# Kernel optimization log

Hardware: AMD Instinct MI355X
Metric: run time of the kernel (lower is better)

## Reference

```python
import jax, jax.numpy as jnp
import numpy as np

D_MODEL = 1024
D_FF = 4096
N_HEADS = 16
D_K = D_MODEL // N_HEADS
EPS = 1e-6
NEG_INF = 1.0e9


def _layer_norm(x, g, b):
    mu = jnp.mean(x, axis=-1, keepdims=True)
    var = jnp.mean(jnp.square(x - mu), axis=-1, keepdims=True)
    return (x - mu) / jnp.sqrt(var + EPS) * g + b


def setup_inputs() -> dict:
    key = jax.random.key(0)
    ks = jax.random.split(key, 16)
    s = 1.0 / np.sqrt(D_MODEL)
    inp = {
        'x': jax.random.normal(ks[0], (4, 2048, D_MODEL), dtype=jnp.float32),
        'e_mask': jnp.ones((4, 1, 2048), dtype=jnp.int32),
        'ln1_g': jnp.ones((D_MODEL,), jnp.float32),
        'ln1_b': jnp.zeros((D_MODEL,), jnp.float32),
        'wq': jax.random.normal(ks[1], (D_MODEL, D_MODEL), jnp.float32) * s,
        'bq': jnp.zeros((D_MODEL,), jnp.float32),
        'wk': jax.random.normal(ks[2], (D_MODEL, D_MODEL), jnp.float32) * s,
        'bk': jnp.zeros((D_MODEL,), jnp.float32),
        'wv': jax.random.normal(ks[3], (D_MODEL, D_MODEL), jnp.float32) * s,
        'bv': jnp.zeros((D_MODEL,), jnp.float32),
        'w0': jax.random.normal(ks[4], (D_MODEL, D_MODEL), jnp.float32) * s,
        'b0': jnp.zeros((D_MODEL,), jnp.float32),
        'ln2_g': jnp.ones((D_MODEL,), jnp.float32),
        'ln2_b': jnp.zeros((D_MODEL,), jnp.float32),
        'w1': jax.random.normal(ks[5], (D_MODEL, D_FF), jnp.float32) * s,
        'b1': jnp.zeros((D_FF,), jnp.float32),
        'w2': jax.random.normal(ks[6], (D_FF, D_MODEL), jnp.float32) * (1.0 / np.sqrt(D_FF)),
        'b2': jnp.zeros((D_MODEL,), jnp.float32),
    }
    return inp


def reference(x, e_mask, ln1_g, ln1_b, wq, bq, wk, bk, wv, bv, w0, b0,
              ln2_g, ln2_b, w1, b1, w2, b2):
    B, S, _ = x.shape
    # --- pre-LN multihead attention (dropout = identity in eval) ---
    x1 = _layer_norm(x, ln1_g, ln1_b)
    q = (x1 @ wq + bq).reshape(B, S, N_HEADS, D_K).transpose(0, 2, 1, 3)
    k = (x1 @ wk + bk).reshape(B, S, N_HEADS, D_K).transpose(0, 2, 1, 3)
    v = (x1 @ wv + bv).reshape(B, S, N_HEADS, D_K).transpose(0, 2, 1, 3)
    scores = jnp.einsum('bhqd,bhkd->bhqk', q, k) / np.sqrt(D_K).astype(np.float32)
    mask = e_mask[:, None, :, :]  # [B,1,1,S] broadcast over heads and queries
    scores = jnp.where(mask == 0, -NEG_INF, scores)
    attn = jax.nn.softmax(scores, axis=-1)
    ctx = jnp.einsum('bhqk,bhkd->bhqd', attn, v)
    ctx = ctx.transpose(0, 2, 1, 3).reshape(B, S, D_MODEL)
    x = x + (ctx @ w0 + b0)
    # --- pre-LN feed-forward ---
    x2 = _layer_norm(x, ln2_g, ln2_b)
    h = jax.nn.relu(x2 @ w1 + b1)
    x = x + (h @ w2 + b2)
    return x
```

## Files before the change

kernel.cpp:

```cpp
#include <hip/hip_runtime.h>
#include <cstdint>
#include <cstddef>

typedef __bf16 bf16;
typedef __bf16 bf16x8 __attribute__((ext_vector_type(8)));
typedef __bf16 bf16x4 __attribute__((ext_vector_type(4)));
typedef float  f32x4  __attribute__((ext_vector_type(4)));
typedef float  f32x16 __attribute__((ext_vector_type(16)));

#define D_MODEL 1024
#define D_FF    4096
#define SEQ     2048
#define NB      4
#define NH      16
#define DKH     64
#define MTOT    (NB * SEQ)

__device__ __forceinline__ void gl_lds16(const void* g, void* l) {
  __builtin_amdgcn_global_load_lds(
      (__attribute__((address_space(1))) unsigned int*)(void*)g,
      (__attribute__((address_space(3))) unsigned int*)l, 16, 0, 0);
}

__device__ __forceinline__ unsigned cvtpk(float lo, float hi_) {
  unsigned r;
  asm("v_cvt_pk_bf16_f32 %0, %1, %2" : "=v"(r) : "v"(lo), "v"(hi_));
  return r;
}
__device__ __forceinline__ void pl32swap(unsigned& a, unsigned& b) {
  asm volatile("v_permlane32_swap_b32 %0, %1" : "+v"(a), "+v"(b));
}

__global__ __launch_bounds__(256) void k_transp(const float* __restrict__ W,
                                                bf16* __restrict__ Wt, int R, int C) {
  __shared__ float tile[32][33];
  const int c0 = blockIdx.x * 32, r0 = blockIdx.y * 32;
  const int t = threadIdx.x;
  const int rl = t >> 5, cl = t & 31;
#pragma unroll
  for (int i = 0; i < 4; ++i)
    tile[rl + i * 8][cl] = W[(size_t)(r0 + rl + i * 8) * C + c0 + cl];
  __syncthreads();
#pragma unroll
  for (int i = 0; i < 4; ++i)
    Wt[(size_t)(c0 + rl + i * 8) * R + r0 + cl] = (bf16)tile[cl][rl + i * 8];
}

__global__ __launch_bounds__(256) void k_ln(const float* __restrict__ x,
                                            const float* __restrict__ g,
                                            const float* __restrict__ b,
                                            bf16* __restrict__ out) {
  const int row = blockIdx.x;
  const int t = threadIdx.x;
  const float4 v = ((const float4*)(x + (size_t)row * D_MODEL))[t];
  float s  = v.x + v.y + v.z + v.w;
  float s2 = v.x * v.x + v.y * v.y + v.z * v.z + v.w * v.w;
#pragma unroll
  for (int off = 1; off < 64; off <<= 1) {
    s  += __shfl_xor(s, off);
    s2 += __shfl_xor(s2, off);
  }
  __shared__ float red[8];
  const int wv = t >> 6;
  if ((t & 63) == 0) { red[wv] = s; red[4 + wv] = s2; }
  __syncthreads();
  s  = red[0] + red[1] + red[2] + red[3];
  s2 = red[4] + red[5] + red[6] + red[7];
  const float mu   = s * (1.f / D_MODEL);
  const float var  = s2 * (1.f / D_MODEL) - mu * mu;
  const float rstd = rsqrtf(var + 1e-6f);
  const float4 gv = ((const float4*)g)[t];
  const float4 bv = ((const float4*)b)[t];
  bf16x4 o;
  o[0] = (bf16)((v.x - mu) * rstd * gv.x + bv.x);
  o[1] = (bf16)((v.y - mu) * rstd * gv.y + bv.y);
  o[2] = (bf16)((v.z - mu) * rstd * gv.z + bv.z);
  o[3] = (bf16)((v.w - mu) * rstd * gv.w + bv.w);
  *(bf16x4*)(out + (size_t)row * D_MODEL + t * 4) = o;
}

template <int EPI>
__global__ __launch_bounds__(512, 2) void k_gemm(
    const bf16* __restrict__ A, const bf16* __restrict__ Bt,
    const float* __restrict__ bias, const float* __restrict__ biasK,
    const float* __restrict__ biasV, float alpha,
    bf16* __restrict__ obf, float* __restrict__ of32,
    const float* __restrict__ resid,
    int M, int N, int K) {
  __shared__ char lds[2][65536];
  const int t = threadIdx.x, lane = t & 63, w = t >> 6;
  const int wm = w >> 2, wn = w & 3;

  const int gx = gridDim.x;
  const int nwg = gx * gridDim.y;
  int id = blockIdx.x + blockIdx.y * gx;
  id = (id & 7) * (nwg >> 3) + (id >> 3);
  const int tn = (id % gx) * 256;
  const int tm = (id / gx) * 256;

  const int scol = 8 * ((lane & 7) ^ (lane >> 3));
  const bf16* aS[4];
  const bf16* bS[4];
#pragma unroll
  for (int i = 0; i < 4; ++i) {
    aS[i] = A  + (size_t)(tm + 8 * (w + 8 * i) + (lane >> 3)) * K + scol;
    bS[i] = Bt + (size_t)(tn + 8 * (w + 8 * i) + (lane >> 3)) * K + scol;
  }
  const int dA = w * 1024;
  const int dB = 32768 + w * 1024;

  const int rA = (wm * 128 + (lane & 15)) * 128;
  const int rB = 32768 + (wn * 64 + (lane & 15)) * 128;
  const int cS0 = (((lane >> 4) * 16)     ) ^ ((lane & 7) << 4);
  const int cS1 = (64 + ((lane >> 4) * 16)) ^ ((lane & 7) << 4);

  f32x4 acc[8][4] = {};
  const int KT = K >> 6;

#pragma unroll
  for (int i = 0; i < 4; ++i) {
    gl_lds16(aS[i], lds[0] + dA + i * 8192);
    gl_lds16(bS[i], lds[0] + dB + i * 8192);
  }
  gl_lds16(aS[0] + 64, lds[1] + dA);
  gl_lds16(aS[1] + 64, lds[1] + dA + 8192);
  asm volatile("s_waitcnt vmcnt(2)" ::: "memory");
  __builtin_amdgcn_s_barrier();
  __builtin_amdgcn_sched_barrier(0);

#define RD(buf, off) (*(const bf16x8*)((buf) + (off)))

  for (int tt = 0; tt < KT; ++tt) {
    char* bufc = lds[tt & 1];
    char* bufn = lds[(tt & 1) ^ 1];
    const int k1 = (tt + 1 < KT ? tt + 1 : KT - 1) * 64;
    const int k2 = (tt + 2 < KT ? tt + 2 : KT - 1) * 64;
    bf16x8 a0[4][2], a1[4][2], b[4][2];
#pragma unroll
    for (int m = 0; m < 4; ++m) {
      a0[m][0] = RD(bufc, rA + m * 2048 + cS0);
      a0[m][1] = RD(bufc, rA + m * 2048 + cS1);
    }
#pragma unroll
    for (int n = 0; n < 2; ++n) {
      b[n][0] = RD(bufc, rB + n * 2048 + cS0);
      b[n][1] = RD(bufc, rB + n * 2048 + cS1);
    }
    gl_lds16(aS[2] + k1, bufn + dA + 2 * 8192);
    gl_lds16(aS[3] + k1, bufn + dA + 3 * 8192);
    gl_lds16(bS[0] + k1, bufn + dB);
    __builtin_amdgcn_s_setprio(1);
#pragma unroll
    for (int m = 0; m < 4; ++m)
#pragma unroll
      for (int n = 0; n < 2; ++n)
#pragma unroll
        for (int s = 0; s < 2; ++s)
          acc[m][n] = __builtin_amdgcn_mfma_f32_16x16x32_bf16(a0[m][s], b[n][s], acc[m][n], 0, 0, 0);
    __builtin_amdgcn_s_setprio(0);
#pragma unroll
    for (int n = 2; n < 4; ++n) {
      b[n][0] = RD(bufc, rB + n * 2048 + cS0);
      b[n][1] = RD(bufc, rB + n * 2048 + cS1);
    }
#pragma unroll
    for (int m = 0; m < 4; ++m) {
      a1[m][0] = RD(bufc, rA + (4 + m) * 2048 + cS0);
      a1[m][1] = RD(bufc, rA + (4 + m) * 2048 + cS1);
    }
    gl_lds16(bS[1] + k1, bufn + dB + 8192);
    gl_lds16(bS[2] + k1, bufn + dB + 2 * 8192);
    gl_lds16(bS[3] + k1, bufn + dB + 3 * 8192);
    __builtin_amdgcn_s_setprio(1);
#pragma unroll
    for (int m = 0; m < 4; ++m)
#pragma unroll
      for (int n = 2; n < 4; ++n)
#pragma unroll
        for (int s = 0; s < 2; ++s)
          acc[m][n] = __builtin_amdgcn_mfma_f32_16x16x32_bf16(a0[m][s], b[n][s], acc[m][n], 0, 0, 0);
    __builtin_amdgcn_s_setprio(0);
    asm volatile("s_waitcnt lgkmcnt(0)" ::: "memory");
    __builtin_amdgcn_s_barrier();
    __builtin_amdgcn_sched_barrier(0);
    gl_lds16(aS[0] + k2, bufc + dA);
    gl_lds16(aS[1] + k2, bufc + dA + 8192);
    __builtin_amdgcn_s_setprio(1);
#pragma unroll
    for (int m = 0; m < 4; ++m)
#pragma unroll
      for (int n = 0; n < 2; ++n)
#pragma unroll
        for (int s = 0; s < 2; ++s)
          acc[4 + m][n] = __builtin_amdgcn_mfma_f32_16x16x32_bf16(a1[m][s], b[n][s], acc[4 + m][n], 0, 0, 0);
    __builtin_amdgcn_s_setprio(0);
    __builtin_amdgcn_s_setprio(1);
#pragma unroll
    for (int m = 0; m < 4; ++m)
#pragma unroll
      for (int n = 2; n < 4; ++n)
#pragma unroll
        for (int s = 0; s < 2; ++s)
          acc[4 + m][n] = __builtin_amdgcn_mfma_f32_16x16x32_bf16(a1[m][s], b[n][s], acc[4 + m][n], 0, 0, 0);
    __builtin_amdgcn_s_setprio(0);
    asm volatile("s_waitcnt vmcnt(2)" ::: "memory");
    __builtin_amdgcn_s_barrier();
    __builtin_amdgcn_sched_barrier(0);
  }
#undef RD
  asm volatile("s_waitcnt vmcnt(0)" ::: "memory");

  const int row0 = tm + wm * 128 + (lane >> 4) * 4;
  const int col0 = tn + wn * 64 + (lane & 15);
  const int which = tn >> 10;
  const float* bp = (EPI == 1) ? (which == 0 ? bias : (which == 1 ? biasK : biasV)) : bias;
  const float af_ = (EPI == 1) ? (which == 0 ? alpha : 1.f) : alpha;
  bf16* qkvB = (EPI == 1) ? obf + (size_t)which * MTOT * D_MODEL : obf;
#pragma unroll
  for (int n = 0; n < 4; ++n) {
    const int col = col0 + n * 16;
    const float bv = (EPI == 1) ? bp[col & 1023] : bp[col];
#pragma unroll
    for (int m = 0; m < 8; ++m) {
#pragma unroll
      for (int r = 0; r < 4; ++r) {
        const int row = row0 + m * 16 + r;
        float val = acc[m][n][r] + bv;
        if constexpr (EPI == 1) {
          const int bb = row >> 11, ss = row & 2047, hh = (col >> 6) & 15, dd = col & 63;
          qkvB[(((size_t)bb * NH + hh) * SEQ + ss) * DKH + dd] = (bf16)(val * af_);
        } else if constexpr (EPI == 2) {
          const size_t idx = (size_t)row * N + col;
          of32[idx] = resid[idx] + val;
        } else {
          obf[(size_t)row * N + col] = (bf16)fmaxf(val, 0.f);
        }
      }
    }
  }
}

template <int EPI>
__global__ __launch_bounds__(512, 2) void k_gemmB(
    const bf16* __restrict__ A, const bf16* __restrict__ Bt,
    const float* __restrict__ bias, float alpha,
    bf16* __restrict__ obf, float* __restrict__ of32,
    const float* __restrict__ resid,
    int M, int N, int K) {
  __shared__ char lds[2][49152];
  const int t = threadIdx.x, lane = t & 63, w = t >> 6;
  const int wm = w >> 1, wn = w & 1;

  const int gx = gridDim.x;
  const int nwg = gx * gridDim.y;
  int id = blockIdx.x + blockIdx.y * gx;
  id = (id & 7) * (nwg >> 3) + (id >> 3);
  const int tn = (id % gx) * 128;
  const int tm = (id / gx) * 256;

  const int srow = w * 16 + (lane >> 3);
  const int scol = 8 * ((lane & 7) ^ (lane >> 3));
  const bf16* aS = A  + (size_t)(tm + srow) * K + scol;
  const bf16* bS = Bt + (size_t)(tn + srow) * K + scol;
  const int dstOff = w * 2048;

  const int rA = (wm * 64 + (lane & 15)) * 128;
  const int rB = 32768 + (wn * 64 + (lane & 15)) * 128;
  const int cS0 = (((lane >> 4) * 16)      ) ^ ((lane & 7) << 4);
  const int cS1 = (64 + ((lane >> 4) * 16) ) ^ ((lane & 7) << 4);

  f32x4 acc[4][4] = {};
  const int KT = K >> 6;

  gl_lds16(aS,                 lds[0] + dstOff);
  gl_lds16(aS + 8 * K,         lds[0] + dstOff + 1024);
  gl_lds16(aS + 128 * K,       lds[0] + 16384 + dstOff);
  gl_lds16(aS + 136 * K,       lds[0] + 16384 + dstOff + 1024);
  gl_lds16(bS,                 lds[0] + 32768 + dstOff);
  gl_lds16(bS + 8 * K,         lds[0] + 32768 + dstOff + 1024);
  gl_lds16(aS + 64,            lds[1] + dstOff);
  gl_lds16(aS + 8 * K + 64,    lds[1] + dstOff + 1024);
  asm volatile("s_waitcnt vmcnt(2)" ::: "memory");
  __builtin_amdgcn_s_barrier();
  __builtin_amdgcn_sched_barrier(0);

#define RD(buf, off) (*(const bf16x8*)((buf) + (off)))
#define MM(m, n, s) acc[m][n] = __builtin_amdgcn_mfma_f32_16x16x32_bf16(a[m][s], b[n][s], acc[m][n], 0, 0, 0)

  for (int tt = 0; tt < KT; ++tt) {
    char* bufc = lds[tt & 1];
    char* bufn = lds[(tt & 1) ^ 1];
    const int k1 = (tt + 1 < KT ? tt + 1 : KT - 1) * 64;
    const int k2 = (tt + 2 < KT ? tt + 2 : KT - 1) * 64;
    bf16x8 a[4][2], b[4][2];
    a[0][0] = RD(bufc, rA + cS0);          a[0][1] = RD(bufc, rA + cS1);
    a[1][0] = RD(bufc, rA + 2048 + cS0);   a[1][1] = RD(bufc, rA + 2048 + cS1);
    b[0][0] = RD(bufc, rB + cS0);
    b[1][0] = RD(bufc, rB + 2048 + cS0);
    b[2][0] = RD(bufc, rB + 4096 + cS0);
    b[3][0] = RD(bufc, rB + 6144 + cS0);
    gl_lds16(aS + 128 * K + k1, bufn + 16384 + dstOff);
    gl_lds16(aS + 136 * K + k1, bufn + 16384 + dstOff + 1024);
    __builtin_amdgcn_s_setprio(1);
    MM(0,0,0); MM(0,1,0); MM(0,2,0); MM(0,3,0);
    MM(1,0,0); MM(1,1,0); MM(1,2,0); MM(1,3,0);
    __builtin_amdgcn_s_setprio(0);
    a[2][0] = RD(bufc, rA + 4096 + cS0);   a[2][1] = RD(bufc, rA + 4096 + cS1);
    a[3][0] = RD(bufc, rA + 6144 + cS0);   a[3][1] = RD(bufc, rA + 6144 + cS1);
    b[0][1] = RD(bufc, rB + cS1);
    b[1][1] = RD(bufc, rB + 2048 + cS1);
    b[2][1] = RD(bufc, rB + 4096 + cS1);
    b[3][1] = RD(bufc, rB + 6144 + cS1);
    gl_lds16(bS + k1,         bufn + 32768 + dstOff);
    gl_lds16(bS + 8 * K + k1, bufn + 32768 + dstOff + 1024);
    __builtin_amdgcn_s_setprio(1);
    MM(2,0,0); MM(2,1,0); MM(2,2,0); MM(2,3,0);
    MM(3,0,0); MM(3,1,0); MM(3,2,0); MM(3,3,0);
    __builtin_amdgcn_s_setprio(0);
    asm volatile("s_waitcnt lgkmcnt(0)" ::: "memory");
    __builtin_amdgcn_s_barrier();
    __builtin_amdgcn_sched_barrier(0);
    gl_lds16(aS + k2,         bufc + dstOff);
    gl_lds16(aS + 8 * K + k2, bufc + dstOff + 1024);
    __builtin_amdgcn_s_setprio(1);
    MM(0,0,1); MM(0,1,1); MM(0,2,1); MM(0,3,1);
    MM(1,0,1); MM(1,1,1); MM(1,2,1); MM(1,3,1);
    __builtin_amdgcn_s_setprio(0);
    __builtin_amdgcn_s_setprio(1);
    MM(2,0,1); MM(2,1,1); MM(2,2,1); MM(2,3,1);
    MM(3,0,1); MM(3,1,1); MM(3,2,1); MM(3,3,1);
    __builtin_amdgcn_s_setprio(0);
    asm volatile("s_waitcnt vmcnt(2)" ::: "memory");
    __builtin_amdgcn_s_barrier();
    __builtin_amdgcn_sched_barrier(0);
  }
#undef RD
#undef MM
  asm volatile("s_waitcnt vmcnt(0)" ::: "memory");

  const int row0 = tm + wm * 64 + (lane >> 4) * 4;
  const int col0 = tn + wn * 64 + (lane & 15);
#pragma unroll
  for (int n = 0; n < 4; ++n) {
    const int col = col0 + n * 16;
    const float bv = bias[col];
#pragma unroll
    for (int m = 0; m < 4; ++m) {
#pragma unroll
      for (int r = 0; r < 4; ++r) {
        const int row = row0 + m * 16 + r;
        float val = acc[m][n][r] + bv;
        if constexpr (EPI == 2) {
          const size_t idx = (size_t)row * N + col;
          of32[idx] = resid[idx] + val;
        } else {
          obf[(size_t)row * N + col] = (bf16)(val * alpha);
        }
      }
    }
  }
}

__global__ __launch_bounds__(256, 4) void k_attn(
    const bf16* __restrict__ q, const bf16* __restrict__ k, const bf16* __restrict__ v,
    const int* __restrict__ emask, bf16* __restrict__ ctx) {
  __shared__ bf16 Kl[64 * 64];
  __shared__ bf16 Vt[64 * 64];
  __shared__ float Msk[64];
  __shared__ int MskFlag;
  const int t = threadIdx.x, lane = t & 63, w = t >> 6;
  const int hi = lane >> 5;
  const int l31 = lane & 31;
  const unsigned swz = (lane & 7) << 4;
  const int bh = blockIdx.x, b = bh >> 4, h = bh & 15;
  const int q0 = blockIdx.y * 128;
  const bf16* qp = q + (size_t)bh * SEQ * DKH;
  const bf16* kp = k + (size_t)bh * SEQ * DKH;
  const bf16* vp = v + (size_t)bh * SEQ * DKH;
  const int* mp = emask + b * SEQ;

  const int qrow = q0 + w * 32 + l31;
  const bf16* qpr = qp + (size_t)qrow * DKH + hi * 8;
  bf16x8 qf[4];
#pragma unroll
  for (int ks = 0; ks < 4; ++ks) qf[ks] = *(const bf16x8*)(qpr + ks * 16);

  const int kcolE = (((lane & 7) * 16) ^ ((lane >> 3) << 4)) >> 1;
  const bf16* kSrc0 = kp + (size_t)(w * 16 + (lane >> 3)) * DKH + kcolE;
  const bf16* kSrc1 = kSrc0 + (size_t)8 * DKH;
  char* kDst0 = (char*)Kl + w * 2048;
  char* kDst1 = kDst0 + 1024;

  const ushort* vU = (const ushort*)vp;
  bf16* vDst0 = (bf16*)((char*)Vt + (lane << 7) + ((w * 32)      ^ ((lane & 7) << 4)));
  bf16* vDst1 = (bf16*)((char*)Vt + (lane << 7) + ((w * 32 + 16) ^ ((lane & 7) << 4)));

  f32x16 O0 = {}, O1 = {};
  float lrun = 0.f;

  for (int kt = 0; kt < SEQ; kt += 64) {
    __syncthreads();
    gl_lds16(kSrc0 + (size_t)kt * DKH, kDst0);
    gl_lds16(kSrc1 + (size_t)kt * DKH, kDst1);
    union { ushort u[8]; bf16x8 v8; } vb0, vb1;
#pragma unroll
    for (int j = 0; j < 8; ++j) {
      vb0.u[j] = vU[(size_t)(kt + w * 16 + j) * 64 + lane];
      vb1.u[j] = vU[(size_t)(kt + w * 16 + 8 + j) * 64 + lane];
    }
    *(bf16x8*)vDst0 = vb0.v8;
    *(bf16x8*)vDst1 = vb1.v8;
    if (t < 64) {
      const float mv = (mp[kt + t] == 0) ? -1e9f : 0.f;
      Msk[t] = mv;
      const unsigned long long bal = __ballot(mv != 0.f);
      if (t == 0) MskFlag = (bal != 0ull);
    }
    __syncthreads();

    f32x16 s0 = {}, s1 = {};
#pragma unroll
    for (int ks = 0; ks < 4; ++ks) {
      const bf16x8 kf = *(const bf16x8*)((const char*)Kl + (l31 << 7) + ((ks * 32 + hi * 16) ^ swz));
      s0 = __builtin_amdgcn_mfma_f32_32x32x16_bf16(kf, qf[ks], s0, 0, 0, 0);
    }
#pragma unroll
    for (int ks = 0; ks < 4; ++ks) {
      const bf16x8 kf = *(const bf16x8*)((const char*)Kl + ((32 + l31) << 7) + ((ks * 32 + hi * 16) ^ swz));
      s1 = __builtin_amdgcn_mfma_f32_32x32x16_bf16(kf, qf[ks], s1, 0, 0, 0);
    }
    if (MskFlag) {
#pragma unroll
      for (int g = 0; g < 4; ++g)
#pragma unroll
        for (int j = 0; j < 4; ++j) {
          s0[g * 4 + j] += Msk[g * 8 + hi * 4 + j];
          s1[g * 4 + j] += Msk[32 + g * 8 + hi * 4 + j];
        }
    }

    float ts = 0.f;
#pragma unroll
    for (int r = 0; r < 16; ++r) { const float p = exp2f(s0[r]); s0[r] = p; ts += p; }
#pragma unroll
    for (int r = 0; r < 16; ++r) { const float p = exp2f(s1[r]); s1[r] = p; ts += p; }
    ts += __shfl_xor(ts, 32);
    lrun += ts;

#define PVSTEP(S, bsel, ks)                                                          \
    {                                                                                \
      unsigned c0 = cvtpk(S[8 * bsel + 0], S[8 * bsel + 1]);                         \
      unsigned c1 = cvtpk(S[8 * bsel + 2], S[8 * bsel + 3]);                         \
      unsigned c2 = cvtpk(S[8 * bsel + 4], S[8 * bsel + 5]);                         \
      unsigned c3 = cvtpk(S[8 * bsel + 6], S[8 * bsel + 7]);                         \
      pl32swap(c0, c2);                                                              \
      pl32swap(c1, c3);                                                              \
      union { unsigned u[4]; bf16x8 vv_; } pu = {{c0, c1, c2, c3}};                  \
      const bf16x8 vf0 = *(const bf16x8*)((const char*)Vt + (l31 << 7) + (((ks) * 32 + hi * 16) ^ swz)); \
      O0 = __builtin_amdgcn_mfma_f32_32x32x16_bf16(vf0, pu.vv_, O0, 0, 0, 0);        \
      const bf16x8 vf1 = *(const bf16x8*)((const char*)Vt + ((32 + l31) << 7) + (((ks) * 32 + hi * 16) ^ swz)); \
      O1 = __builtin_amdgcn_mfma_f32_32x32x16_bf16(vf1, pu.vv_, O1, 0, 0, 0);        \
    }
    PVSTEP(s0, 0, 0)
    PVSTEP(s0, 1, 1)
    PVSTEP(s1, 0, 2)
    PVSTEP(s1, 1, 3)
#undef PVSTEP
  }

  const float rl = 1.f / lrun;
  bf16* cp = ctx + ((size_t)b * SEQ + qrow) * D_MODEL + h * 64;
#pragma unroll
  for (int r = 0; r < 16; ++r) {
    const int d0 = (r & 3) + 8 * (r >> 2) + hi * 4;
    cp[d0]      = (bf16)(O0[r] * rl);
    cp[32 + d0] = (bf16)(O1[r] * rl);
  }
}

extern "C" void kernel_launch(void* const* d_in, const int* in_sizes, int n_in,
                              void* d_out, int out_size, void* d_ws, size_t ws_size,
                              hipStream_t stream) {
  (void)in_sizes; (void)n_in; (void)out_size; (void)ws_size;
  const float* x    = (const float*)d_in[0];
  const int*   em   = (const int*)d_in[1];
  const float* ln1g = (const float*)d_in[2];
  const float* ln1b = (const float*)d_in[3];
  const float* wq   = (const float*)d_in[4];
  const float* bq   = (const float*)d_in[5];
  const float* wk   = (const float*)d_in[6];
  const float* bk   = (const float*)d_in[7];
  const float* wv   = (const float*)d_in[8];
  const float* bv   = (const float*)d_in[9];
  const float* w0   = (const float*)d_in[10];
  const float* b0   = (const float*)d_in[11];
  const float* ln2g = (const float*)d_in[12];
  const float* ln2b = (const float*)d_in[13];
  const float* w1   = (const float*)d_in[14];
  const float* b1   = (const float*)d_in[15];
  const float* w2   = (const float*)d_in[16];
  const float* b2   = (const float*)d_in[17];
  float* out = (float*)d_out;

  char* ws = (char*)d_ws;
  const size_t MB = 1u << 20;
  bf16* wqT = (bf16*)(ws + 0 * MB);
  bf16* w0T = (bf16*)(ws + 6 * MB);
  bf16* w1T = (bf16*)(ws + 8 * MB);
  bf16* w2T = (bf16*)(ws + 16 * MB);
  bf16* x1  = (bf16*)(ws + 24 * MB);
  bf16* qB  = (bf16*)(ws + 40 * MB);
  bf16* kB  = (bf16*)(ws + 56 * MB);
  bf16* vB  = (bf16*)(ws + 72 * MB);
  bf16* cB  = (bf16*)(ws + 88 * MB);
  bf16* hB  = (bf16*)(ws + 40 * MB);

  k_transp<<<dim3(32, 32),  256, 0, stream>>>(wq, wqT,                   1024, 1024);
  k_transp<<<dim3(32, 32),  256, 0, stream>>>(wk, wqT + 1024 * 1024,     1024, 1024);
  k_transp<<<dim3(32, 32),  256, 0, stream>>>(wv, wqT + 2 * 1024 * 1024, 1024, 1024);
  k_transp<<<dim3(32, 32),  256, 0, stream>>>(w0, w0T, 1024, 1024);
  k_transp<<<dim3(128, 32), 256, 0, stream>>>(w1, w1T, 1024, 4096);
  k_transp<<<dim3(32, 128), 256, 0, stream>>>(w2, w2T, 4096, 1024);

  k_ln<<<MTOT, 256, 0, stream>>>(x, ln1g, ln1b, x1);

  k_gemm<1><<<dim3(12, MTOT / 256), 512, 0, stream>>>(
      x1, wqT, bq, bk, bv, 0.125f * 1.44269504f, qB, nullptr, nullptr, MTOT, 3072, 1024);

  k_attn<<<dim3(64, 16), 256, 0, stream>>>(qB, kB, vB, em, cB);

  k_gemmB<2><<<dim3(8, MTOT / 256), 512, 0, stream>>>(
      cB, w0T, b0, 1.0f, nullptr, out, x, MTOT, 1024, 1024);

  k_ln<<<MTOT, 256, 0, stream>>>(out, ln2g, ln2b, x1);

  k_gemm<3><<<dim3(16, MTOT / 256), 512, 0, stream>>>(
      x1, w1T, b1, nullptr, nullptr, 1.0f, hB, nullptr, nullptr, MTOT, 4096, 1024);

  k_gemmB<2><<<dim3(8, MTOT / 256), 512, 0, stream>>>(
      hB, w2T, b2, 1.0f, nullptr, out, out, MTOT, 1024, 4096);
}
```

Before: 542.2 us.

## Double-buffer K/V/mask tiles in attention kernel to overlap loads with MFMA

The attention kernel now keeps two LDS buffers for the K tile, the transposed V tile and the mask. It prefetches the next tile's K (via global_load_lds), V (into registers) and mask while computing on the current one, and drops one barrier per iteration. The goal is to hide global load latency behind the QK and PV MFMA work. In exchange, LDS use per block doubles to about 33KB, which may limit occupancy, and V is held in registers across the compute phase, which adds register pressure.

Measured after the change: 526.7 us. -2.9%, faster.

```diff
diff --git a/kernel.cpp b/kernel.cpp
--- a/kernel.cpp
+++ b/kernel.cpp
@@ -364,10 +364,10 @@
 __global__ __launch_bounds__(256, 4) void k_attn(
     const bf16* __restrict__ q, const bf16* __restrict__ k, const bf16* __restrict__ v,
     const int* __restrict__ emask, bf16* __restrict__ ctx) {
-  __shared__ bf16 Kl[64 * 64];
-  __shared__ bf16 Vt[64 * 64];
-  __shared__ float Msk[64];
-  __shared__ int MskFlag;
+  __shared__ bf16 Kl[2][64 * 64];
+  __shared__ bf16 Vt[2][64 * 64];
+  __shared__ float Msk[2][64];
+  __shared__ int MskFlag[2];
   const int t = threadIdx.x, lane = t & 63, w = t >> 6;
   const int hi = lane >> 5;
   const int l31 = lane & 31;
@@ -388,54 +388,69 @@
   const int kcolE = (((lane & 7) * 16) ^ ((lane >> 3) << 4)) >> 1;
   const bf16* kSrc0 = kp + (size_t)(w * 16 + (lane >> 3)) * DKH + kcolE;
   const bf16* kSrc1 = kSrc0 + (size_t)8 * DKH;
-  char* kDst0 = (char*)Kl + w * 2048;
-  char* kDst1 = kDst0 + 1024;
+  const int kOff0 = w * 2048, kOff1 = w * 2048 + 1024;
 
   const ushort* vU = (const ushort*)vp;
-  bf16* vDst0 = (bf16*)((char*)Vt + (lane << 7) + ((w * 32)      ^ ((lane & 7) << 4)));
-  bf16* vDst1 = (bf16*)((char*)Vt + (lane << 7) + ((w * 32 + 16) ^ ((lane & 7) << 4)));
+  const int vOff0 = (lane << 7) + ((w * 32)      ^ ((lane & 7) << 4));
+  const int vOff1 = (lane << 7) + ((w * 32 + 16) ^ ((lane & 7) << 4));
 
   f32x16 O0 = {}, O1 = {};
   float lrun = 0.f;
+  union { ushort u[8]; bf16x8 v8; } vb0, vb1;
+
+  gl_lds16(kSrc0, (char*)Kl[0] + kOff0);
+  gl_lds16(kSrc1, (char*)Kl[0] + kOff1);
+#pragma unroll
+  for (int j = 0; j < 8; ++j) {
+    vb0.u[j] = vU[(size_t)(w * 16 + j) * 64 + lane];
+    vb1.u[j] = vU[(size_t)(w * 16 + 8 + j) * 64 + lane];
+  }
+  if (t < 64) {
+    const float mv = (mp[t] == 0) ? -1e9f : 0.f;
+    Msk[0][t] = mv;
+    const unsigned long long bal = __ballot(mv != 0.f);
+    if (t == 0) MskFlag[0] = (bal != 0ull);
+  }
+  asm volatile("s_waitcnt vmcnt(0)" ::: "memory");
+  *(bf16x8*)((char*)Vt[0] + vOff0) = vb0.v8;
+  *(bf16x8*)((char*)Vt[0] + vOff1) = vb1.v8;
+  __syncthreads();
 
   for (int kt = 0; kt < SEQ; kt += 64) {
-    __syncthreads();
-    gl_lds16(kSrc0 + (size_t)kt * DKH, kDst0);
-    gl_lds16(kSrc1 + (size_t)kt * DKH, kDst1);
-    union { ushort u[8]; bf16x8 v8; } vb0, vb1;
+    const int cur = (kt >> 6) & 1, nxt = cur ^ 1;
+    const int ktn = (kt + 64 < SEQ) ? kt + 64 : kt;
+    gl_lds16(kSrc0 + (size_t)ktn * DKH, (char*)Kl[nxt] + kOff0);
+    gl_lds16(kSrc1 + (size_t)ktn * DKH, (char*)Kl[nxt] + kOff1);
 #pragma unroll
     for (int j = 0; j < 8; ++j) {
-      vb0.u[j] = vU[(size_t)(kt + w * 16 + j) * 64 + lane];
-      vb1.u[j] = vU[(size_t)(kt + w * 16 + 8 + j) * 64 + lane];
-    }
-    *(bf16x8*)vDst0 = vb0.v8;
-    *(bf16x8*)vDst1 = vb1.v8;
+      vb0.u[j] = vU[(size_t)(ktn + w * 16 + j) * 64 + lane];
+      vb1.u[j] = vU[(size_t)(ktn + w * 16 + 8 + j) * 64 + lane];
+    }
     if (t < 64) {
-      const float mv = (mp[kt + t] == 0) ? -1e9f : 0.f;
-      Msk[t] = mv;
+      const float mv = (mp[ktn + t] == 0) ? -1e9f : 0.f;
+      Msk[nxt][t] = mv;
       const unsigned long long bal = __ballot(mv != 0.f);
-      if (t == 0) MskFlag = (bal != 0ull);
-    }
-    __syncthreads();
+      if (t == 0) MskFlag[nxt] = (bal != 0ull);
+    }
 
     f32x16 s0 = {}, s1 = {};
 #pragma unroll
     for (int ks = 0; ks < 4; ++ks) {
-      const bf16x8 kf = *(const bf16x8*)((const char*)Kl + (l31 << 7) + ((ks * 32 + hi * 16) ^ swz));
+      const bf16x8 kf = *(const bf16x8*)((const char*)Kl[cur] + (l31 << 7) + ((ks * 32 + hi * 16) ^ swz));
       s0 = __builtin_amdgcn_mfma_f32_32x32x16_bf16(kf, qf[ks], s0, 0, 0, 0);
     }
 #pragma unroll
     for (int ks = 0; ks < 4; ++ks) {
-      const bf16x8 kf = *(const bf16x8*)((const char*)Kl + ((32 + l31) << 7) + ((ks * 32 + hi * 16) ^ swz));
+      const bf16x8 kf = *(const bf16x8*)((const char*)Kl[cur] + ((32 + l31) << 7) + ((ks * 32 + hi * 16) ^ swz));
       s1 = __builtin_amdgcn_mfma_f32_32x32x16_bf16(kf, qf[ks], s1, 0, 0, 0);
     }
-    if (MskFlag) {
+    if (MskFlag[cur]) {
 #pragma unroll
       for (int g = 0; g < 4; ++g)
 #pragma unroll
         for (int j = 0; j < 4; ++j) {
-          s0[g * 4 + j] += Msk[g * 8 + hi * 4 + j];
-          s1[g * 4 + j] += Msk[32 + g * 8 + hi * 4 + j];
+          s0[g * 4 + j] += Msk[cur][g * 8 + hi * 4 + j];
+          s1[g * 4 + j] += Msk[cur][32 + g * 8 + hi * 4 + j];
         }
     }
 
@@ -456,9 +471,9 @@
       pl32swap(c0, c2);                                                              \
       pl32swap(c1, c3);                                                              \
       union { unsigned u[4]; bf16x8 vv_; } pu = {{c0, c1, c2, c3}};                  \
-      const bf16x8 vf0 = *(const bf16x8*)((const char*)Vt + (l31 << 7) + (((ks) * 32 + hi * 16) ^ swz)); \
+      const bf16x8 vf0 = *(const bf16x8*)((const char*)Vt[cur] + (l31 << 7) + (((ks) * 32 + hi * 16) ^ swz)); \
       O0 = __builtin_amdgcn_mfma_f32_32x32x16_bf16(vf0, pu.vv_, O0, 0, 0, 0);        \
-      const bf16x8 vf1 = *(const bf16x8*)((const char*)Vt + ((32 + l31) << 7) + (((ks) * 32 + hi * 16) ^ swz)); \
+      const bf16x8 vf1 = *(const bf16x8*)((const char*)Vt[cur] + ((32 + l31) << 7) + (((ks) * 32 + hi * 16) ^ swz)); \
       O1 = __builtin_amdgcn_mfma_f32_32x32x16_bf16(vf1, pu.vv_, O1, 0, 0, 0);        \
     }
     PVSTEP(s0, 0, 0)
@@ -466,6 +481,11 @@
     PVSTEP(s1, 0, 2)
     PVSTEP(s1, 1, 3)
 #undef PVSTEP
+
+    asm volatile("s_waitcnt vmcnt(0)" ::: "memory");
+    *(bf16x8*)((char*)Vt[nxt] + vOff0) = vb0.v8;
+    *(bf16x8*)((char*)Vt[nxt] + vOff1) = vb1.v8;
+    __syncthreads();
   }
 
   const float rl = 1.f / lrun;
```
